# Optimization experiments

Hardware: AMD Instinct MI355X
Metric: run time of the kernel (lower is better)

Reference implementation:

```python
import jax, jax.numpy as jnp
import numpy as np

B, S, D, H = 2, 2048, 1024, 16
HD = D // H  # head_dim = 64


def setup_inputs() -> dict:
    key = jax.random.key(0)
    k1, k2, k3 = jax.random.split(key, 3)
    x = jax.random.normal(k1, (B, S, D), dtype=jnp.float32)
    mask = jnp.zeros((B, S, S), dtype=jnp.float32)  # additive mask
    # Dense(3*D) params (glorot-ish scale) and Dense(D) output projection
    Wqkv = jax.random.normal(k2, (D, 3 * D), dtype=jnp.float32) * (1.0 / np.sqrt(D))
    bqkv = jnp.zeros((3 * D,), dtype=jnp.float32)
    Wo = jax.random.normal(k3, (D, D), dtype=jnp.float32) * (1.0 / np.sqrt(D))
    bo = jnp.zeros((D,), dtype=jnp.float32)
    return {"x": x, "mask": mask, "Wqkv": Wqkv, "bqkv": bqkv, "Wo": Wo, "bo": bo}


def reference(x, mask, Wqkv, bqkv, Wo, bo):
    b, s, d = x.shape
    qkv = x @ Wqkv + bqkv                              # [B,S,3D]
    qkv = qkv.reshape(b, s, H, 3 * HD).transpose(0, 2, 1, 3)  # [B,H,S,3*HD]
    q, k, v = jnp.split(qkv, 3, axis=-1)               # each [B,H,S,HD]
    scale = 1.0 / jnp.sqrt(jnp.float32(HD))
    scores = jnp.einsum('bhqd,bhkd->bhqk', q, k) * scale  # [B,H,S,S]
    scores = scores + mask[:, None, :, :]
    attn = jax.nn.softmax(scores, axis=-1)
    values = jnp.einsum('bhqk,bhkd->bhqd', attn, v)    # [B,H,S,HD]
    # Faithful to original: reshape WITHOUT transposing heads back
    values = values.reshape(b, s, H * HD)              # [B,S,D]
    return values @ Wo + bo
```

## Files before the change

kernel.cpp:

```cpp
#include <hip/hip_runtime.h>
#include <hip/hip_bf16.h>

#define B_ 2
#define S_ 2048
#define D_ 1024
#define H_ 16
#define HD_ 64

typedef __attribute__((ext_vector_type(8))) short short8;
typedef __attribute__((ext_vector_type(4))) float f32x4;
typedef __attribute__((ext_vector_type(16))) float f32x16;
typedef __attribute__((ext_vector_type(4))) unsigned short us4;

static __device__ __forceinline__ ushort f2bf(float x) {
  __hip_bfloat16 h = __float2bfloat16(x);
  return *reinterpret_cast<ushort*>(&h);
}

static __device__ __forceinline__ void gld_lds16(void* lds, const void* g) {
  __builtin_amdgcn_global_load_lds(
      (__attribute__((address_space(1))) void*)(g),
      (__attribute__((address_space(3))) void*)(lds), 16, 0, 0);
}


__global__ __launch_bounds__(256) void cvt_bf16_vec(const float4* __restrict__ in,
                                                    ushort* __restrict__ out, int n4) {
  int i = blockIdx.x * blockDim.x + threadIdx.x;
  if (i < n4) {
    float4 v = in[i];
    ushort4 o;
    o.x = f2bf(v.x); o.y = f2bf(v.y); o.z = f2bf(v.z); o.w = f2bf(v.w);
    *reinterpret_cast<ushort4*>(out + (size_t)i * 4) = o;
  }
}

__global__ __launch_bounds__(256) void transpose_cvt(const float* __restrict__ in,
                                                     ushort* __restrict__ out,
                                                     int K, int N) {
  __shared__ float tile[32][33];
  const int bn = blockIdx.x * 32, bk = blockIdx.y * 32;
  const int tx = threadIdx.x, ty = threadIdx.y;
  #pragma unroll
  for (int i = ty; i < 32; i += 8)
    tile[i][tx] = in[(size_t)(bk + i) * N + bn + tx];
  __syncthreads();
  #pragma unroll
  for (int i = ty; i < 32; i += 8)
    out[(size_t)(bn + i) * K + bk + tx] = f2bf(tile[tx][i]);
}

template <bool OUT_BF16>
__global__ __launch_bounds__(256) void gemm_bt(const ushort* __restrict__ A,
                                               const ushort* __restrict__ Bt,
                                               const float* __restrict__ bias,
                                               ushort* __restrict__ Cb,
                                               float* __restrict__ Cf,
                                               int M, int N, int K) {
  __shared__ __align__(16) ushort As[128 * 32];
  __shared__ __align__(16) ushort Bs[128 * 32];
  const int tid = threadIdx.x;
  const int lane = tid & 63, wid = tid >> 6;
  const int wr = wid >> 1, wc = wid & 1;
  const int row0 = blockIdx.x * 128, col0 = blockIdx.y * 128;
  const int l15 = lane & 15, lhi = lane >> 4;

  f32x4 acc[4][4];
  #pragma unroll
  for (int i = 0; i < 4; ++i)
    #pragma unroll
    for (int j = 0; j < 4; ++j)
      acc[i][j] = f32x4{0.f, 0.f, 0.f, 0.f};

  const int sr = tid >> 2;
  const int scol = (tid & 3) * 8;

  for (int k0 = 0; k0 < K; k0 += 32) {
    gld_lds16(&As[(size_t)tid * 8],        &A[(size_t)(row0 + sr) * K + k0 + scol]);
    gld_lds16(&As[2048 + (size_t)tid * 8], &A[(size_t)(row0 + 64 + sr) * K + k0 + scol]);
    gld_lds16(&Bs[(size_t)tid * 8],        &Bt[(size_t)(col0 + sr) * K + k0 + scol]);
    gld_lds16(&Bs[2048 + (size_t)tid * 8], &Bt[(size_t)(col0 + 64 + sr) * K + k0 + scol]);
    __syncthreads();

    short8 af[4], bfr[4];
    #pragma unroll
    for (int mt = 0; mt < 4; ++mt)
      af[mt] = *(const short8*)&As[(wr * 64 + mt * 16 + l15) * 32 + lhi * 8];
    #pragma unroll
    for (int nt = 0; nt < 4; ++nt)
      bfr[nt] = *(const short8*)&Bs[(wc * 64 + nt * 16 + l15) * 32 + lhi * 8];
    #pragma unroll
    for (int mt = 0; mt < 4; ++mt)
      #pragma unroll
      for (int nt = 0; nt < 4; ++nt)
        acc[mt][nt] = __builtin_amdgcn_mfma_f32_16x16x32_bf16(af[mt], bfr[nt], acc[mt][nt], 0, 0, 0);
    __syncthreads();
  }

  const int orow = row0 + wr * 64;
  const int ocol = col0 + wc * 64 + l15;
  #pragma unroll
  for (int mt = 0; mt < 4; ++mt) {
    #pragma unroll
    for (int nt = 0; nt < 4; ++nt) {
      const int gc = ocol + nt * 16;
      const float bv = bias[gc];
      #pragma unroll
      for (int r = 0; r < 4; ++r) {
        const int gr = orow + mt * 16 + lhi * 4 + r;
        const float v = acc[mt][nt][r] + bv;
        if (OUT_BF16) Cb[(size_t)gr * N + gc] = f2bf(v);
        else          Cf[(size_t)gr * N + gc] = v;
      }
    }
  }
}

__global__ __launch_bounds__(256, 2) void flash_attn(const ushort* __restrict__ qkv,
                                                     const float* __restrict__ mask,
                                                     ushort* __restrict__ values) {
  __shared__ __align__(16) ushort Ks[2][2][64 * 64];
  __shared__ __align__(16) ushort Vt[2][2][64 * 64];

  const int tid = threadIdx.x;
  const int lane = tid & 63, wid = tid >> 6;
  const int l31 = lane & 31, lhalf = lane >> 5;
  const int qt = blockIdx.x, bh = blockIdx.y, b = bh >> 4, h = bh & 15;
  const size_t base = (size_t)b * S_ * 3072 + (size_t)h * 192;
  const int q = qt * 128 + wid * 32 + l31;

  short8 qf[4];
  {
    const ushort* qrow = qkv + base + (size_t)q * 3072 + lhalf * 8;
    qf[0] = *(const short8*)(qrow);
    qf[1] = *(const short8*)(qrow + 16);
    qf[2] = *(const short8*)(qrow + 32);
    qf[3] = *(const short8*)(qrow + 48);
  }

  const int srow = tid >> 3, sch = tid & 7;
  const int hsr = (srow ^ (srow >> 3)) & 7;
  const int scs = sch ^ hsr;
  const int kg = tid & 15, d0 = (tid >> 4) * 4;
  const int skg = (kg & 12) | ((kg & 1) << 1) | ((kg >> 1) & 1);

  float m_run = -3.0e38f, l_run = 0.f;
  f32x16 o[2];
  #pragma unroll
  for (int dg = 0; dg < 2; ++dg)
    #pragma unroll
    for (int i = 0; i < 16; ++i) o[dg][i] = 0.f;

  const float* mrow = mask + ((size_t)b * S_ + q) * S_;
  const int NT2 = S_ / 128;
  int cur = 0;
  us4 vr[8];

  {
    #pragma unroll
    for (int s2 = 0; s2 < 2; ++s2) {
      const ushort* kgp = qkv + base + (size_t)(s2 * 64 + srow) * 3072 + 64;
      gld_lds16(&Ks[0][s2][tid * 8],        kgp + scs * 8);
      gld_lds16(&Ks[0][s2][2048 + tid * 8], kgp + (size_t)32 * 3072 + (scs ^ 4) * 8);
      #pragma unroll
      for (int kk = 0; kk < 4; ++kk)
        vr[s2 * 4 + kk] = *(const us4*)(qkv + base +
                           (size_t)(s2 * 64 + kg * 4 + kk) * 3072 + 128 + d0);
    }
    #pragma unroll
    for (int s2 = 0; s2 < 2; ++s2)
      #pragma unroll
      for (int dd = 0; dd < 4; ++dd) {
        const int d = d0 + dd;
        const int hd = (d ^ (d >> 3)) & 7;
        us4 w;
        w[0] = vr[s2 * 4 + 0][dd]; w[1] = vr[s2 * 4 + 1][dd];
        w[2] = vr[s2 * 4 + 2][dd]; w[3] = vr[s2 * 4 + 3][dd];
        *(us4*)&Vt[0][s2][d * 64 + (((skg >> 1) ^ hd) & 7) * 8 + (skg & 1) * 4] = w;
      }
    __syncthreads();
  }

  for (int t = 0; t < NT2; ++t) {
    const int nxt = cur ^ 1;
    const bool pre = (t + 1 < NT2);

    f32x4 mk[16];
    {
      const float* mp0 = mrow + (size_t)t * 128 + lhalf * 4;
      #pragma unroll
      for (int i = 0; i < 16; ++i)
        mk[i] = *(const f32x4*)(mp0 + (i >> 3) * 64 + ((i >> 2) & 1) * 32 + (i & 3) * 8);
    }

    if (pre) {
      const size_t nb = base + (size_t)(t + 1) * 128 * 3072;
      #pragma unroll
      for (int s2 = 0; s2 < 2; ++s2) {
        const ushort* kgp = qkv + nb + (size_t)(s2 * 64 + srow) * 3072 + 64;
        gld_lds16(&Ks[nxt][s2][tid * 8],        kgp + scs * 8);
        gld_lds16(&Ks[nxt][s2][2048 + tid * 8], kgp + (size_t)32 * 3072 + (scs ^ 4) * 8);
        #pragma unroll
        for (int kk = 0; kk < 4; ++kk)
          vr[s2 * 4 + kk] = *(const us4*)(qkv + nb +
                             (size_t)(s2 * 64 + kg * 4 + kk) * 3072 + 128 + d0);
      }
    }

    f32x16 sc[4];
    __builtin_amdgcn_s_setprio(1);
    #pragma unroll
    for (int s2 = 0; s2 < 2; ++s2)
      #pragma unroll
      for (int g = 0; g < 2; ++g) {
        const int row = g * 32 + l31;
        const int hk = (row ^ (row >> 3)) & 7;
        const ushort* kp = &Ks[cur][s2][row * 64];
        f32x16 s;
        #pragma unroll
        for (int i = 0; i < 16; ++i) s[i] = 0.f;
        #pragma unroll
        for (int kd = 0; kd < 4; ++kd) {
          short8 kf = *(const short8*)&kp[(((kd * 2 + lhalf) ^ hk) & 7) * 8];
          s = __builtin_amdgcn_mfma_f32_32x32x16_bf16(kf, qf[kd], s, 0, 0, 0);
        }
        sc[s2 * 2 + g] = s;
      }
    __builtin_amdgcn_s_setprio(0);

    #pragma unroll
    for (int c4 = 0; c4 < 4; ++c4)
      #pragma unroll
      for (int r = 0; r < 16; ++r)
        sc[c4][r] = sc[c4][r] * 0.125f + mk[(c4 >> 1) * 8 + (c4 & 1) * 4 + (r >> 2)][r & 3];

    float mx = sc[0][0];
    #pragma unroll
    for (int c4 = 0; c4 < 4; ++c4)
      #pragma unroll
      for (int r = 0; r < 16; ++r) mx = fmaxf(mx, sc[c4][r]);
    mx = fmaxf(mx, __shfl_xor(mx, 32));
    if (__any(mx > m_run + 8.0f)) {
      const float mnew = fmaxf(m_run, mx);
      const float alpha = __expf(m_run - mnew);
      m_run = mnew;
      l_run *= alpha;
      #pragma unroll
      for (int dg = 0; dg < 2; ++dg)
        #pragma unroll
        for (int i = 0; i < 16; ++i) o[dg][i] *= alpha;
    }
    float ps = 0.f;
    #pragma unroll
    for (int c4 = 0; c4 < 4; ++c4)
      #pragma unroll
      for (int r = 0; r < 16; ++r) {
        const float p = __expf(sc[c4][r] - m_run);
        sc[c4][r] = p;
        ps += p;
      }
    ps += __shfl_xor(ps, 32);
    l_run += ps;

    short8 pf[8];
    #pragma unroll
    for (int ks = 0; ks < 8; ++ks) {
      const int sub = ks >> 2, k2 = ks & 3;
      #pragma unroll
      for (int j = 0; j < 8; ++j)
        pf[ks][j] = (short)f2bf(sc[sub * 2 + (k2 >> 1)][8 * (k2 & 1) + j]);
    }

    __builtin_amdgcn_s_setprio(1);
    #pragma unroll
    for (int dg = 0; dg < 2; ++dg) {
      const int d = dg * 32 + l31;
      const int hv = (d ^ (d >> 3)) & 7;
      #pragma unroll
      for (int ks = 0; ks < 8; ++ks) {
        const int sub = ks >> 2, kl = ks & 3;
        const ushort* vp = &Vt[cur][sub][d * 64];
        short8 vf = *(const short8*)&vp[(((kl * 2 + lhalf) ^ hv) & 7) * 8];
        o[dg] = __builtin_amdgcn_mfma_f32_32x32x16_bf16(vf, pf[ks], o[dg], 0, 0, 0);
      }
    }
    __builtin_amdgcn_s_setprio(0);

    if (pre) {
      #pragma unroll
      for (int s2 = 0; s2 < 2; ++s2)
        #pragma unroll
        for (int dd = 0; dd < 4; ++dd) {
          const int d = d0 + dd;
          const int hd = (d ^ (d >> 3)) & 7;
          us4 w;
          w[0] = vr[s2 * 4 + 0][dd]; w[1] = vr[s2 * 4 + 1][dd];
          w[2] = vr[s2 * 4 + 2][dd]; w[3] = vr[s2 * 4 + 3][dd];
          *(us4*)&Vt[nxt][s2][d * 64 + (((skg >> 1) ^ hd) & 7) * 8 + (skg & 1) * 4] = w;
        }
    }
    __syncthreads();
    cur = nxt;
  }

  const float inv = 1.0f / l_run;
  ushort* vout = values + ((size_t)bh * S_ + q) * 64;
  #pragma unroll
  for (int dg = 0; dg < 2; ++dg)
    #pragma unroll
    for (int quad = 0; quad < 4; ++quad) {
      us4 w;
      #pragma unroll
      for (int r = 0; r < 4; ++r) w[r] = f2bf(o[dg][quad * 4 + r] * inv);
      *(us4*)(vout + dg * 32 + quad * 8 + lhalf * 4) = w;
    }
}


extern "C" void kernel_launch(void* const* d_in, const int* in_sizes, int n_in,
                              void* d_out, int out_size, void* d_ws, size_t ws_size,
                              hipStream_t stream) {
  const float* x    = (const float*)d_in[0];
  const float* mask = (const float*)d_in[1];
  const float* Wqkv = (const float*)d_in[2];
  const float* bqkv = (const float*)d_in[3];
  const float* Wo   = (const float*)d_in[4];
  const float* bo   = (const float*)d_in[5];
  float* out = (float*)d_out;

  char* ws = (char*)d_ws;
  ushort* xbf    = (ushort*)(ws + 0);
  ushort* vals   = (ushort*)(ws + 0);
  ushort* wqkvT  = (ushort*)(ws + 8388608);
  ushort* woT    = (ushort*)(ws + 14680064);
  ushort* qkv    = (ushort*)(ws + 16777216);

  cvt_bf16_vec<<<4096, 256, 0, stream>>>((const float4*)x, xbf, (B_ * S_ * D_) / 4);
  transpose_cvt<<<dim3(3 * D_ / 32, D_ / 32), dim3(32, 8), 0, stream>>>(Wqkv, wqkvT, D_, 3 * D_);
  transpose_cvt<<<dim3(D_ / 32, D_ / 32), dim3(32, 8), 0, stream>>>(Wo, woT, D_, D_);
  gemm_bt<true><<<dim3((B_ * S_) / 128, (3 * D_) / 128), 256, 0, stream>>>(
      xbf, wqkvT, bqkv, qkv, nullptr, B_ * S_, 3 * D_, D_);
  flash_attn<<<dim3(S_ / 128, B_ * H_), 256, 0, stream>>>(qkv, mask, vals);
  gemm_bt<false><<<dim3((B_ * S_) / 128, D_ / 128), 256, 0, stream>>>(
      vals, woT, bo, nullptr, out, B_ * S_, D_, D_);
}
```

Measured before the change: 196.7 us.

## Split attention tile into two 64-key halves and stage K through registers

The per-tile softmax and PV loop now runs in two 64-key sub-steps, each with its own max, exp and PV MFMA, so fewer score registers are live at once. K prefetch changes from direct global-to-LDS loads to register loads that are written to LDS after compute, like V. The mask load moves after the prefetch issue. This trades lower register pressure and possibly better overlap for extra online-softmax rescale checks and more VGPRs held for the K prefetch.

```diff
diff --git a/kernel.cpp b/kernel.cpp
--- a/kernel.cpp
+++ b/kernel.cpp
@@ -154,6 +154,7 @@
   const float* mrow = mask + ((size_t)b * S_ + q) * S_;
   const int NT2 = S_ / 128;
   int cur = 0;
+  short8 kr[4];
   us4 vr[8];
 
   {
@@ -185,32 +186,36 @@
     const int nxt = cur ^ 1;
     const bool pre = (t + 1 < NT2);
 
-    f32x4 mk[16];
-    {
-      const float* mp0 = mrow + (size_t)t * 128 + lhalf * 4;
-      #pragma unroll
-      for (int i = 0; i < 16; ++i)
-        mk[i] = *(const f32x4*)(mp0 + (i >> 3) * 64 + ((i >> 2) & 1) * 32 + (i & 3) * 8);
-    }
-
     if (pre) {
       const size_t nb = base + (size_t)(t + 1) * 128 * 3072;
-      #pragma unroll
-      for (int s2 = 0; s2 < 2; ++s2) {
-        const ushort* kgp = qkv + nb + (size_t)(s2 * 64 + srow) * 3072 + 64;
-        gld_lds16(&Ks[nxt][s2][tid * 8],        kgp + scs * 8);
-        gld_lds16(&Ks[nxt][s2][2048 + tid * 8], kgp + (size_t)32 * 3072 + (scs ^ 4) * 8);
+      kr[0] = *(const short8*)(qkv + nb + (size_t)(srow)      * 3072 + 64 + scs * 8);
+      kr[1] = *(const short8*)(qkv + nb + (size_t)(32 + srow) * 3072 + 64 + (scs ^ 4) * 8);
+      kr[2] = *(const short8*)(qkv + nb + (size_t)(64 + srow) * 3072 + 64 + scs * 8);
+      kr[3] = *(const short8*)(qkv + nb + (size_t)(96 + srow) * 3072 + 64 + (scs ^ 4) * 8);
+      #pragma unroll
+      for (int s2 = 0; s2 < 2; ++s2)
         #pragma unroll
         for (int kk = 0; kk < 4; ++kk)
           vr[s2 * 4 + kk] = *(const us4*)(qkv + nb +
                              (size_t)(s2 * 64 + kg * 4 + kk) * 3072 + 128 + d0);
-      }
-    }
-
-    f32x16 sc[4];
-    __builtin_amdgcn_s_setprio(1);
-    #pragma unroll
-    for (int s2 = 0; s2 < 2; ++s2)
+    }
+    f32x4 mka[8], mkb[8];
+    {
+      const float* mp = mrow + (size_t)t * 128 + lhalf * 4;
+      #pragma unroll
+      for (int i = 0; i < 8; ++i)
+        mka[i] = *(const f32x4*)(mp + (i >> 2) * 32 + (i & 3) * 8);
+      #pragma unroll
+      for (int i = 0; i < 8; ++i)
+        mkb[i] = *(const f32x4*)(mp + 64 + (i >> 2) * 32 + (i & 3) * 8);
+    }
+
+    #pragma unroll
+    for (int s2 = 0; s2 < 2; ++s2) {
+      const f32x4* mk = (s2 == 0) ? mka : mkb;
+
+      f32x16 sc[2];
+      __builtin_amdgcn_s_setprio(1);
       #pragma unroll
       for (int g = 0; g < 2; ++g) {
         const int row = g * 32 + l31;
@@ -224,69 +229,71 @@
           short8 kf = *(const short8*)&kp[(((kd * 2 + lhalf) ^ hk) & 7) * 8];
           s = __builtin_amdgcn_mfma_f32_32x32x16_bf16(kf, qf[kd], s, 0, 0, 0);
         }
-        sc[s2 * 2 + g] = s;
-      }
-    __builtin_amdgcn_s_setprio(0);
-
-    #pragma unroll
-    for (int c4 = 0; c4 < 4; ++c4)
-      #pragma unroll
-      for (int r = 0; r < 16; ++r)
-        sc[c4][r] = sc[c4][r] * 0.125f + mk[(c4 >> 1) * 8 + (c4 & 1) * 4 + (r >> 2)][r & 3];
-
-    float mx = sc[0][0];
-    #pragma unroll
-    for (int c4 = 0; c4 < 4; ++c4)
-      #pragma unroll
-      for (int r = 0; r < 16; ++r) mx = fmaxf(mx, sc[c4][r]);
-    mx = fmaxf(mx, __shfl_xor(mx, 32));
-    if (__any(mx > m_run + 8.0f)) {
-      const float mnew = fmaxf(m_run, mx);
-      const float alpha = __expf(m_run - mnew);
-      m_run = mnew;
-      l_run *= alpha;
-      #pragma unroll
-      for (int dg = 0; dg < 2; ++dg)
-        #pragma unroll
-        for (int i = 0; i < 16; ++i) o[dg][i] *= alpha;
-    }
-    float ps = 0.f;
-    #pragma unroll
-    for (int c4 = 0; c4 < 4; ++c4)
-      #pragma unroll
-      for (int r = 0; r < 16; ++r) {
-        const float p = __expf(sc[c4][r] - m_run);
-        sc[c4][r] = p;
-        ps += p;
-      }
-    ps += __shfl_xor(ps, 32);
-    l_run += ps;
-
-    short8 pf[8];
-    #pragma unroll
-    for (int ks = 0; ks < 8; ++ks) {
-      const int sub = ks >> 2, k2 = ks & 3;
-      #pragma unroll
-      for (int j = 0; j < 8; ++j)
-        pf[ks][j] = (short)f2bf(sc[sub * 2 + (k2 >> 1)][8 * (k2 & 1) + j]);
-    }
-
-    __builtin_amdgcn_s_setprio(1);
-    #pragma unroll
-    for (int dg = 0; dg < 2; ++dg) {
-      const int d = dg * 32 + l31;
-      const int hv = (d ^ (d >> 3)) & 7;
-      #pragma unroll
-      for (int ks = 0; ks < 8; ++ks) {
-        const int sub = ks >> 2, kl = ks & 3;
-        const ushort* vp = &Vt[cur][sub][d * 64];
-        short8 vf = *(const short8*)&vp[(((kl * 2 + lhalf) ^ hv) & 7) * 8];
-        o[dg] = __builtin_amdgcn_mfma_f32_32x32x16_bf16(vf, pf[ks], o[dg], 0, 0, 0);
-      }
-    }
-    __builtin_amdgcn_s_setprio(0);
+        sc[g] = s;
+      }
+      __builtin_amdgcn_s_setprio(0);
+
+      #pragma unroll
+      for (int g = 0; g < 2; ++g)
+        #pragma unroll
+        for (int r = 0; r < 16; ++r)
+          sc[g][r] = sc[g][r] * 0.125f + mk[g * 4 + (r >> 2)][r & 3];
+
+      float mx = sc[0][0];
+      #pragma unroll
+      for (int g = 0; g < 2; ++g)
+        #pragma unroll
+        for (int r = 0; r < 16; ++r) mx = fmaxf(mx, sc[g][r]);
+      mx = fmaxf(mx, __shfl_xor(mx, 32));
+      if (__any(mx > m_run + 8.0f)) {
+        const float mnew = fmaxf(m_run, mx);
+        const float alpha = __expf(m_run - mnew);
+        m_run = mnew;
+        l_run *= alpha;
+        #pragma unroll
+        for (int dg = 0; dg < 2; ++dg)
+          #pragma unroll
+          for (int i = 0; i < 16; ++i) o[dg][i] *= alpha;
+      }
+      float ps = 0.f;
+      #pragma unroll
+      for (int g = 0; g < 2; ++g)
+        #pragma unroll
+        for (int r = 0; r < 16; ++r) {
+          const float p = __expf(sc[g][r] - m_run);
+          sc[g][r] = p;
+          ps += p;
+        }
+      ps += __shfl_xor(ps, 32);
+      l_run += ps;
+
+      short8 pf[4];
+      #pragma unroll
+      for (int ks = 0; ks < 4; ++ks)
+        #pragma unroll
+        for (int j = 0; j < 8; ++j)
+          pf[ks][j] = (short)f2bf(sc[ks >> 1][8 * (ks & 1) + j]);
+
+      __builtin_amdgcn_s_setprio(1);
+      #pragma unroll
+      for (int dg = 0; dg < 2; ++dg) {
+        const int d = dg * 32 + l31;
+        const int hv = (d ^ (d >> 3)) & 7;
+        const ushort* vp = &Vt[cur][s2][d * 64];
+        #pragma unroll
+        for (int ks = 0; ks < 4; ++ks) {
+          short8 vf = *(const short8*)&vp[(((ks * 2 + lhalf) ^ hv) & 7) * 8];
+          o[dg] = __builtin_amdgcn_mfma_f32_32x32x16_bf16(vf, pf[ks], o[dg], 0, 0, 0);
+        }
+      }
+      __builtin_amdgcn_s_setprio(0);
+    }
 
     if (pre) {
+      *(short8*)&Ks[nxt][0][tid * 8]        = kr[0];
+      *(short8*)&Ks[nxt][0][2048 + tid * 8] = kr[1];
+      *(short8*)&Ks[nxt][1][tid * 8]        = kr[2];
+      *(short8*)&Ks[nxt][1][2048 + tid * 8] = kr[3];
       #pragma unroll
       for (int s2 = 0; s2 < 2; ++s2)
         #pragma unroll
```

After: 189.4 us. 3.7% less time.
